# Optimization experiments

Measured on AMD Instinct MI355X. Metric: run time of the kernel, lower is better.

## Reference

```python
import jax, jax.numpy as jnp
import numpy as np

N = 100000      # nodes
E = 1600000     # edges (avg degree 16)
IN = 128
HID = 128
OUT = 128
G = 512         # graphs in batch


def setup_inputs() -> dict:
    key = jax.random.key(0)
    ks = jax.random.split(key, 8)
    x = jax.random.normal(ks[0], (N, IN), dtype=jnp.float32)
    edge_index = jax.random.randint(ks[1], (2, E), 0, N, dtype=jnp.int64)
    batch = jnp.sort(jax.random.randint(ks[2], (N,), 0, G, dtype=jnp.int64))
    # GCNConv params: weight (glorot-ish) + zero bias, per layer
    W1 = jax.random.normal(ks[3], (IN, HID), dtype=jnp.float32) / np.sqrt(IN)
    b1 = jnp.zeros((HID,), jnp.float32)
    W2 = jax.random.normal(ks[4], (HID, OUT), dtype=jnp.float32) / np.sqrt(HID)
    b2 = jnp.zeros((OUT,), jnp.float32)
    return {"x": x, "edge_index": edge_index, "batch": batch,
            "W1": W1, "b1": b1, "W2": W2, "b2": b2}


def _gcn_layer(h, W, b, src, dst, norm, n):
    # linear transform then normalized scatter-add aggregation
    h = h @ W                                  # [N, F_out]
    msg = h[src] * norm[:, None]               # [E+N, F_out]
    out = jax.ops.segment_sum(msg, dst, num_segments=n)
    return out + b


def reference(x, edge_index, batch, W1, b1, W2, b2):
    x = x.astype(jnp.float32)
    n = x.shape[0]
    # GCNConv adds self-loops and uses symmetric deg^-1/2 normalization
    loop = jnp.arange(n)
    src = jnp.concatenate([edge_index[0], loop])
    dst = jnp.concatenate([edge_index[1], loop])
    deg = jax.ops.segment_sum(jnp.ones_like(dst, dtype=x.dtype), dst, num_segments=n)
    dis = jnp.where(deg > 0, jax.lax.rsqrt(jnp.maximum(deg, 1.0)), 0.0)
    norm = dis[src] * dis[dst]                 # [E+N]

    h = jax.nn.relu(_gcn_layer(x, W1, b1, src, dst, norm, n))
    # dropout p=0.0 -> identity
    h = jax.nn.relu(_gcn_layer(h, W2, b2, src, dst, norm, n))

    # global_mean_pool over batch ids
    sums = jax.ops.segment_sum(h, batch, num_segments=G)          # [G, OUT]
    counts = jax.ops.segment_sum(jnp.ones((n,), h.dtype), batch, num_segments=G)
    return sums / jnp.maximum(counts, 1.0)[:, None]
```

## Files before the change

kernel.cpp:

```cpp
#include <hip/hip_runtime.h>
#include <stddef.h>


#define F 128
#define EB 4096
#define BSH 9

typedef unsigned int uint;
typedef unsigned short ushort;
typedef __attribute__((ext_vector_type(8))) short s16x8;
typedef __attribute__((ext_vector_type(4))) float f32x4;

__device__ __forceinline__ float bf_lo(uint v) { return __uint_as_float(v << 16); }
__device__ __forceinline__ float bf_hi(uint v) { return __uint_as_float(v & 0xffff0000u); }
__device__ __forceinline__ ushort f2bf(float f) {
    uint u = __float_as_uint(f);
    u += 0x7fffu + ((u >> 16) & 1u);
    return (ushort)(u >> 16);
}
__device__ __forceinline__ uint pack_bf2(float lo, float hi) {
    return (uint)f2bf(lo) | ((uint)f2bf(hi) << 16);
}

__device__ __forceinline__ int scan256_incl(int* s, int t, int v) {
    s[t] = v;
    __syncthreads();
#pragma unroll
    for (int d = 1; d < 256; d <<= 1) {
        int y = (t >= d) ? s[t - d] : 0;
        __syncthreads();
        s[t] += y;
        __syncthreads();
    }
    return s[t];
}


__global__ __launch_bounds__(256) void passA_kernel(const int* __restrict__ ei,
                                                    int* __restrict__ bucket_cnt,
                                                    int e, int nbuc) {
    __shared__ int h[256];
    int t = threadIdx.x;
    h[t] = 0;
    __syncthreads();
    for (int i = blockIdx.x * 256 + t; i < e; i += gridDim.x * 256)
        atomicAdd(&h[ei[e + i] >> BSH], 1);
    __syncthreads();
    if (t < nbuc && h[t]) atomicAdd(&bucket_cnt[t], h[t]);
}


__global__ __launch_bounds__(256) void prep_scan_kernel(const float* __restrict__ W1,
                                                        const float* __restrict__ W2,
                                                        ushort* __restrict__ wt,
                                                        const int* __restrict__ bucket_cnt,
                                                        int* __restrict__ bucket_base,
                                                        int* __restrict__ gcur, int nbuc) {
    if (blockIdx.x == 128) {
        __shared__ int aux[256];
        int t = threadIdx.x;
        int v = (t < nbuc) ? bucket_cnt[t] : 0;
        int incl = scan256_incl(aux, t, v);
        int base = incl - v;
        bucket_base[t] = base;
        gcur[t] = base;
        if (t == nbuc - 1) bucket_base[nbuc] = incl;
        return;
    }
    int idx = blockIdx.x * 256 + threadIdx.x;
    int m = idx >> 14;
    int c = (idx >> 7) & 127;
    int r = idx & 127;
    const float* W = m ? W2 : W1;
    float w = W[r * F + c];
    ushort hi = f2bf(w);
    float whi = __uint_as_float((uint)hi << 16);
    ushort lo = f2bf(w - whi);
    wt[((m * 2 + 0) * F + c) * F + r] = hi;
    wt[((m * 2 + 1) * F + c) * F + r] = lo;
}


__global__ __launch_bounds__(256) void passB_kernel(const int* __restrict__ ei,
                                                    int* __restrict__ gcur,
                                                    uint2* __restrict__ ebuf, int e) {
    __shared__ uint2 stage[EB];
    __shared__ int h[256], start[256], cur[256], claim[256], aux[256];
    int t = threadIdx.x;
    h[t] = 0;
    __syncthreads();
    int base = blockIdx.x * EB;
    int s_r[16], d_r[16];
#pragma unroll
    for (int k = 0; k < 16; ++k) {
        int i = base + k * 256 + t;
        int sv = -1, dv = 0;
        if (i < e) {
            sv = ei[i];
            dv = ei[e + i];
            atomicAdd(&h[dv >> BSH], 1);
        }
        s_r[k] = sv; d_r[k] = dv;
    }
    __syncthreads();
    int hv = h[t];
    int incl = scan256_incl(aux, t, hv);
    start[t] = incl - hv;
    cur[t]   = incl - hv;
    claim[t] = (hv > 0) ? atomicAdd(&gcur[t], hv) : 0;
    __syncthreads();
#pragma unroll
    for (int k = 0; k < 16; ++k) {
        if (s_r[k] >= 0) {
            int b = d_r[k] >> BSH;
            int r = atomicAdd(&cur[b], 1);
            stage[r] = make_uint2((uint)s_r[k], (uint)d_r[k]);
        }
    }
    __syncthreads();
    int valid = min(EB, e - base);
#pragma unroll
    for (int k = 0; k < 16; ++k) {
        int idx = k * 256 + t;
        if (idx < valid) {
            uint2 ed = stage[idx];
            int b = (int)(ed.y >> BSH);
            ebuf[claim[b] + (idx - start[b])] = ed;
        }
    }
}


__global__ __launch_bounds__(256) void passC1_kernel(const uint2* __restrict__ ebuf,
                                                     const int* __restrict__ bucket_base,
                                                     int* __restrict__ rp,
                                                     float* __restrict__ dis, int n) {
    __shared__ int h[512];
    __shared__ int aux[256];
    int t = threadIdx.x, b = blockIdx.x;
    int v0 = b << BSH;
    h[t] = 0; h[t + 256] = 0;
    __syncthreads();
    int ebeg = bucket_base[b], eend = bucket_base[b + 1];
    for (int i = ebeg + t; i < eend; i += 256)
        atomicAdd(&h[(int)ebuf[i].y - v0], 1);
    __syncthreads();
#pragma unroll
    for (int k = 0; k < 2; ++k) {
        int v = v0 + t + k * 256;
        if (v < n) dis[v] = rsqrtf((float)(h[t + k * 256] + 1));
    }
    int p = h[2 * t] + h[2 * t + 1];
    int incl = scan256_incl(aux, t, p);
    int ex = incl - p;
    int v = v0 + 2 * t;
    if (v <= n)     rp[v]     = ebeg + ex;
    if (v + 1 <= n) rp[v + 1] = ebeg + ex + h[2 * t];
}


__global__ __launch_bounds__(256) void passC2_kernel(const uint2* __restrict__ ebuf,
                                                     const int* __restrict__ bucket_base,
                                                     const int* __restrict__ rp,
                                                     const float* __restrict__ dis,
                                                     uint2* __restrict__ ew, int n) {
    __shared__ int cur[512];
    __shared__ float dl[512];
    int t = threadIdx.x, b = blockIdx.x;
    int v0 = b << BSH;
#pragma unroll
    for (int k = 0; k < 2; ++k) {
        int idx = t + k * 256, v = v0 + idx;
        cur[idx] = (v < n) ? rp[v] : 0;
        dl[idx]  = (v < n) ? dis[v] : 0.f;
    }
    __syncthreads();
    int ebeg = bucket_base[b], eend = bucket_base[b + 1];
    for (int i = ebeg + t; i < eend; i += 256) {
        uint2 ed = ebuf[i];
        int s = (int)ed.x, d = (int)ed.y - v0;
        float w = dis[s] * dl[d];
        int p = atomicAdd(&cur[d], 1);
        ew[p] = make_uint2(ed.x, __float_as_uint(w));
    }
}


template <bool F32IN>
__global__ __launch_bounds__(256) void gemm_mfma_kernel(const float* __restrict__ Af,
                                                        const uint* __restrict__ Ab,
                                                        const ushort* __restrict__ wt,
                                                        ushort* __restrict__ C,
                                                        int n, int nstrips) {
    __shared__ uint4 As4[2][2048];
    const int t = threadIdx.x;
    const int w = t >> 6;
    const int lane = t & 63;
    const int kg = lane >> 4;
    const int lr = lane & 15;

    const uint4* Bg = (const uint4*)wt;
    s16x8 bfr[2][2][4];
#pragma unroll
    for (int part = 0; part < 2; ++part)
#pragma unroll
        for (int c = 0; c < 2; ++c)
#pragma unroll
            for (int ks = 0; ks < 4; ++ks) {
                int col = w * 32 + c * 16 + lr;
                uint4 bu = Bg[part * F * 16 + col * 16 + ks * 4 + kg];
                bfr[part][c][ks] = *(const s16x8*)&bu;
            }

    auto load_strip = [&](int strip, uint4* st) {
        int r0 = strip * 128;
#pragma unroll
        for (int p = 0; p < 8; ++p) {
            int g = p * 256 + t;
            int row = g >> 4, q = g & 15;
            int c8 = q ^ (row & 7);
            uint4 v = make_uint4(0u, 0u, 0u, 0u);
            int gr = r0 + row;
            if (gr < n) {
                if (F32IN) {
                    const float* a = Af + (size_t)gr * F + c8 * 8;
                    float4 f0 = *(const float4*)a;
                    float4 f1 = *(const float4*)(a + 4);
                    v.x = pack_bf2(f0.x, f0.y);
                    v.y = pack_bf2(f0.z, f0.w);
                    v.z = pack_bf2(f1.x, f1.y);
                    v.w = pack_bf2(f1.z, f1.w);
                } else {
                    v = *(const uint4*)(Ab + (size_t)gr * 64 + c8 * 4);
                }
            }
            st[p] = v;
        }
    };

    int s = blockIdx.x;
    if (s >= nstrips) return;
    uint4 st[8];
    load_strip(s, st);
    int buf = 0;
    for (; s < nstrips; s += gridDim.x) {
#pragma unroll
        for (int p = 0; p < 8; ++p) As4[buf][p * 256 + t] = st[p];
        __syncthreads();
        int s2 = s + gridDim.x;
        if (s2 < nstrips) load_strip(s2, st);

        f32x4 acc[8][2];
#pragma unroll
        for (int r = 0; r < 8; ++r)
#pragma unroll
            for (int c = 0; c < 2; ++c) acc[r][c] = (f32x4){0.f, 0.f, 0.f, 0.f};

        const s16x8* As8 = (const s16x8*)As4[buf];
#pragma unroll
        for (int ks = 0; ks < 4; ++ks) {
            s16x8 afr[8];
#pragma unroll
            for (int r = 0; r < 8; ++r) {
                int row = r * 16 + lr;
                afr[r] = As8[row * 16 + ((ks * 4 + kg) ^ (row & 7))];
            }
#pragma unroll
            for (int r = 0; r < 8; ++r)
#pragma unroll
                for (int c = 0; c < 2; ++c) {
                    acc[r][c] = __builtin_amdgcn_mfma_f32_16x16x32_bf16(afr[r], bfr[0][c][ks], acc[r][c], 0, 0, 0);
                    acc[r][c] = __builtin_amdgcn_mfma_f32_16x16x32_bf16(afr[r], bfr[1][c][ks], acc[r][c], 0, 0, 0);
                }
        }
        __syncthreads();

        ushort* Cs = (ushort*)As4[buf];
#pragma unroll
        for (int r = 0; r < 8; ++r)
#pragma unroll
            for (int c = 0; c < 2; ++c)
#pragma unroll
                for (int reg = 0; reg < 4; ++reg) {
                    int row = r * 16 + kg * 4 + reg;
                    int col = w * 32 + c * 16 + lr;
                    Cs[row * F + col] = f2bf(acc[r][c][reg]);
                }
        __syncthreads();
        int r0 = s * 128;
#pragma unroll
        for (int p = 0; p < 8; ++p) {
            int g = p * 256 + t;
            int row = g >> 4, c8 = g & 15;
            if (r0 + row < n)
                *(uint4*)(C + (size_t)(r0 + row) * F + c8 * 8) = As4[buf][g];
        }
        buf ^= 1;
    }
}


__global__ __launch_bounds__(256) void agg_kernel(const uint* __restrict__ h2,
                                                  const int* __restrict__ rp,
                                                  const uint2* __restrict__ ew,
                                                  const float* __restrict__ dis,
                                                  const float* __restrict__ bias,
                                                  uint* __restrict__ out2, int n) {
    int wid = __builtin_amdgcn_readfirstlane(threadIdx.x >> 6);
    int node = blockIdx.x * 4 + wid;
    if (node >= n) return;
    int lane = threadIdx.x & 63;
    float di = dis[node];
    int beg = rp[node], end = rp[node + 1];
    uint hv = h2[((uint)node << 6) | lane];
    float w0 = di * di;
    float ax = w0 * bf_lo(hv);
    float ay = w0 * bf_hi(hv);
    int j = beg;
    for (; j + 16 <= end; j += 16) {
        uint2 E[16];
        uint v[16];
#pragma unroll
        for (int k = 0; k < 16; ++k) E[k] = ew[j + k];
#pragma unroll
        for (int k = 0; k < 16; ++k) v[k] = h2[(E[k].x << 6) | lane];
#pragma unroll
        for (int k = 0; k < 16; ++k) {
            float we = __uint_as_float(E[k].y);
            ax = fmaf(we, bf_lo(v[k]), ax);
            ay = fmaf(we, bf_hi(v[k]), ay);
        }
    }
    for (; j + 4 <= end; j += 4) {
        uint2 E0 = ew[j], E1 = ew[j + 1], E2 = ew[j + 2], E3 = ew[j + 3];
        uint v0 = h2[(E0.x << 6) | lane];
        uint v1 = h2[(E1.x << 6) | lane];
        uint v2 = h2[(E2.x << 6) | lane];
        uint v3 = h2[(E3.x << 6) | lane];
        float w0e = __uint_as_float(E0.y), w1e = __uint_as_float(E1.y);
        float w2e = __uint_as_float(E2.y), w3e = __uint_as_float(E3.y);
        ax = fmaf(w0e, bf_lo(v0), ax); ay = fmaf(w0e, bf_hi(v0), ay);
        ax = fmaf(w1e, bf_lo(v1), ax); ay = fmaf(w1e, bf_hi(v1), ay);
        ax = fmaf(w2e, bf_lo(v2), ax); ay = fmaf(w2e, bf_hi(v2), ay);
        ax = fmaf(w3e, bf_lo(v3), ax); ay = fmaf(w3e, bf_hi(v3), ay);
    }
    for (; j < end; ++j) {
        uint2 E0 = ew[j];
        uint v0 = h2[(E0.x << 6) | lane];
        float w0e = __uint_as_float(E0.y);
        ax = fmaf(w0e, bf_lo(v0), ax);
        ay = fmaf(w0e, bf_hi(v0), ay);
    }
    float2 b = ((const float2*)bias)[lane];
    ax = fmaxf(ax + b.x, 0.f);
    ay = fmaxf(ay + b.y, 0.f);
    out2[((uint)node << 6) | lane] = pack_bf2(ax, ay);
}


__global__ __launch_bounds__(256) void pool_kernel(const uint* __restrict__ h2,
                                                   const int* __restrict__ batch,
                                                   float* __restrict__ out, int n) {
    __shared__ int sb[2];
    __shared__ float red[4][F];
    int g = blockIdx.x;
    int t = threadIdx.x;
    if (t < 2) {
        int target = g + t;
        int lo = 0, hi = n;
        while (lo < hi) {
            int mid = (lo + hi) >> 1;
            if (batch[mid] < target) lo = mid + 1; else hi = mid;
        }
        sb[t] = lo;
    }
    __syncthreads();
    int start = sb[0], end = sb[1];
    int lane = t & 63, w = t >> 6;
    float sx = 0.f, sy = 0.f;
    for (int i = start + w; i < end; i += 4) {
        uint v = h2[((uint)i << 6) | lane];
        sx += bf_lo(v);
        sy += bf_hi(v);
    }
    red[w][lane * 2] = sx;
    red[w][lane * 2 + 1] = sy;
    __syncthreads();
    if (w == 0) {
        float s0 = red[0][lane * 2] + red[1][lane * 2] + red[2][lane * 2] + red[3][lane * 2];
        float s1 = red[0][lane * 2 + 1] + red[1][lane * 2 + 1] + red[2][lane * 2 + 1] + red[3][lane * 2 + 1];
        float inv = 1.f / fmaxf((float)(end - start), 1.f);
        out[(size_t)g * F + lane * 2]     = s0 * inv;
        out[(size_t)g * F + lane * 2 + 1] = s1 * inv;
    }
}


extern "C" void kernel_launch(void* const* d_in, const int* in_sizes, int n_in,
                              void* d_out, int out_size, void* d_ws, size_t ws_size,
                              hipStream_t stream) {
    const float* x     = (const float*)d_in[0];
    const int*   ei    = (const int*)d_in[1];
    const int*   batch = (const int*)d_in[2];
    const float* W1    = (const float*)d_in[3];
    const float* b1    = (const float*)d_in[4];
    const float* W2    = (const float*)d_in[5];
    const float* b2    = (const float*)d_in[6];
    float* out = (float*)d_out;

    const int n = in_sizes[0] / F;
    const int e = in_sizes[1] / 2;
    const int g = out_size / F;
    const int nbuc = (n + (1 << BSH) - 1) >> BSH;

    char* ws = (char*)d_ws;
    size_t off = 0;
    auto alloc = [&](size_t bytes) -> char* {
        char* p = ws + off;
        off += (bytes + 255) & ~(size_t)255;
        return p;
    };
    float*  dis   = (float*)alloc((size_t)n * 4);
    int*    rp    = (int*)  alloc((size_t)(n + 1) * 4);
    int*    bcnt  = (int*)  alloc(256 * 4);
    int*    bbase = (int*)  alloc(257 * 4);
    int*    gcur  = (int*)  alloc(256 * 4);
    uint2*  ebuf  = (uint2*)alloc((size_t)e * 8);
    uint2*  ew    = (uint2*)alloc((size_t)e * 8);
    ushort* wt    = (ushort*)alloc((size_t)4 * F * F * 2);
    uint*   hbuf  = (uint*) alloc((size_t)n * F * 2);
    uint*   abuf  = (uint*) alloc((size_t)n * F * 2);
    (void)ws_size;

    hipMemsetAsync(bcnt, 0, 256 * 4, stream);
    passA_kernel<<<256, 256, 0, stream>>>(ei, bcnt, e, nbuc);
    prep_scan_kernel<<<129, 256, 0, stream>>>(W1, W2, wt, bcnt, bbase, gcur, nbuc);
    passB_kernel<<<(e + EB - 1) / EB, 256, 0, stream>>>(ei, gcur, ebuf, e);
    passC1_kernel<<<nbuc, 256, 0, stream>>>(ebuf, bbase, rp, dis, n);
    passC2_kernel<<<nbuc, 256, 0, stream>>>(ebuf, bbase, rp, dis, ew, n);

    const int nstrips = (n + 127) / 128;
    int ggrid = nstrips < 512 ? nstrips : 512;
    gemm_mfma_kernel<true><<<ggrid, 256, 0, stream>>>(x, nullptr, wt, (ushort*)hbuf, n, nstrips);
    agg_kernel<<<(n + 3) / 4, 256, 0, stream>>>(hbuf, rp, ew, dis, b1, abuf, n);
    gemm_mfma_kernel<false><<<ggrid, 256, 0, stream>>>(nullptr, abuf, wt + 2 * F * F, (ushort*)hbuf, n, nstrips);
    agg_kernel<<<(n + 3) / 4, 256, 0, stream>>>(hbuf, rp, ew, dis, b2, abuf, n);
    pool_kernel<<<g, 256, 0, stream>>>(abuf, batch, out, n);
}
```

Baseline: 349.8 us.

## Pack edge buffer to 32-bit, shrink buckets, one-strip-per-block GEMM

```diff
diff --git a/kernel.cpp b/kernel.cpp
--- a/kernel.cpp
+++ b/kernel.cpp
@@ -4,7 +4,7 @@
 
 #define F 128
 #define EB 4096
-#define BSH 9
+#define BSH 8
 
 typedef unsigned int uint;
 typedef unsigned short ushort;
@@ -39,14 +39,18 @@
 __global__ __launch_bounds__(256) void passA_kernel(const int* __restrict__ ei,
                                                     int* __restrict__ bucket_cnt,
                                                     int e, int nbuc) {
-    __shared__ int h[256];
+    __shared__ int h[512];
     int t = threadIdx.x;
-    h[t] = 0;
+    h[t] = 0; h[t + 256] = 0;
     __syncthreads();
     for (int i = blockIdx.x * 256 + t; i < e; i += gridDim.x * 256)
         atomicAdd(&h[ei[e + i] >> BSH], 1);
     __syncthreads();
-    if (t < nbuc && h[t]) atomicAdd(&bucket_cnt[t], h[t]);
+#pragma unroll
+    for (int k = 0; k < 2; ++k) {
+        int b = t + k * 256;
+        if (b < nbuc && h[b]) atomicAdd(&bucket_cnt[b], h[b]);
+    }
 }
 
 
@@ -59,12 +63,16 @@
     if (blockIdx.x == 128) {
         __shared__ int aux[256];
         int t = threadIdx.x;
-        int v = (t < nbuc) ? bucket_cnt[t] : 0;
-        int incl = scan256_incl(aux, t, v);
-        int base = incl - v;
-        bucket_base[t] = base;
-        gcur[t] = base;
-        if (t == nbuc - 1) bucket_base[nbuc] = incl;
+        int c0 = (2 * t < nbuc) ? bucket_cnt[2 * t] : 0;
+        int c1 = (2 * t + 1 < nbuc) ? bucket_cnt[2 * t + 1] : 0;
+        int p = c0 + c1;
+        int incl = scan256_incl(aux, t, p);
+        int ex = incl - p;
+        bucket_base[2 * t] = ex;
+        bucket_base[2 * t + 1] = ex + c0;
+        gcur[2 * t] = ex;
+        gcur[2 * t + 1] = ex + c0;
+        if (t == 255) bucket_base[512] = incl;
         return;
     }
     int idx = blockIdx.x * 256 + threadIdx.x;
@@ -83,11 +91,11 @@
 
 __global__ __launch_bounds__(256) void passB_kernel(const int* __restrict__ ei,
                                                     int* __restrict__ gcur,
-                                                    uint2* __restrict__ ebuf, int e) {
+                                                    uint* __restrict__ ebuf, int e) {
     __shared__ uint2 stage[EB];
-    __shared__ int h[256], start[256], cur[256], claim[256], aux[256];
+    __shared__ int h[512], start[512], cur[512], claim[512], aux[256];
     int t = threadIdx.x;
-    h[t] = 0;
+    h[t] = 0; h[t + 256] = 0;
     __syncthreads();
     int base = blockIdx.x * EB;
     int s_r[16], d_r[16];
@@ -103,11 +111,16 @@
         s_r[k] = sv; d_r[k] = dv;
     }
     __syncthreads();
-    int hv = h[t];
-    int incl = scan256_incl(aux, t, hv);
-    start[t] = incl - hv;
-    cur[t]   = incl - hv;
-    claim[t] = (hv > 0) ? atomicAdd(&gcur[t], hv) : 0;
+    {
+        int h0 = h[2 * t], h1 = h[2 * t + 1];
+        int p = h0 + h1;
+        int incl = scan256_incl(aux, t, p);
+        int ex = incl - p;
+        start[2 * t] = ex;          start[2 * t + 1] = ex + h0;
+        cur[2 * t] = ex;            cur[2 * t + 1] = ex + h0;
+        claim[2 * t]     = (h0 > 0) ? atomicAdd(&gcur[2 * t], h0) : 0;
+        claim[2 * t + 1] = (h1 > 0) ? atomicAdd(&gcur[2 * t + 1], h1) : 0;
+    }
     __syncthreads();
 #pragma unroll
     for (int k = 0; k < 16; ++k) {
@@ -125,63 +138,58 @@
         if (idx < valid) {
             uint2 ed = stage[idx];
             int b = (int)(ed.y >> BSH);
-            ebuf[claim[b] + (idx - start[b])] = ed;
-        }
-    }
-}
-
-
-__global__ __launch_bounds__(256) void passC1_kernel(const uint2* __restrict__ ebuf,
+            uint dloc = ed.y & ((1u << BSH) - 1u);
+            ebuf[claim[b] + (idx - start[b])] = (dloc << 24) | ed.x;
+        }
+    }
+}
+
+
+__global__ __launch_bounds__(256) void passC1_kernel(const uint* __restrict__ ebuf,
                                                      const int* __restrict__ bucket_base,
                                                      int* __restrict__ rp,
                                                      float* __restrict__ dis, int n) {
-    __shared__ int h[512];
+    __shared__ int h[256];
     __shared__ int aux[256];
     int t = threadIdx.x, b = blockIdx.x;
     int v0 = b << BSH;
-    h[t] = 0; h[t + 256] = 0;
+    h[t] = 0;
     __syncthreads();
     int ebeg = bucket_base[b], eend = bucket_base[b + 1];
     for (int i = ebeg + t; i < eend; i += 256)
-        atomicAdd(&h[(int)ebuf[i].y - v0], 1);
-    __syncthreads();
-#pragma unroll
-    for (int k = 0; k < 2; ++k) {
-        int v = v0 + t + k * 256;
-        if (v < n) dis[v] = rsqrtf((float)(h[t + k * 256] + 1));
-    }
-    int p = h[2 * t] + h[2 * t + 1];
-    int incl = scan256_incl(aux, t, p);
-    int ex = incl - p;
-    int v = v0 + 2 * t;
-    if (v <= n)     rp[v]     = ebeg + ex;
-    if (v + 1 <= n) rp[v + 1] = ebeg + ex + h[2 * t];
-}
-
-
-__global__ __launch_bounds__(256) void passC2_kernel(const uint2* __restrict__ ebuf,
+        atomicAdd(&h[ebuf[i] >> 24], 1);
+    __syncthreads();
+    int cnt = h[t];
+    int v = v0 + t;
+    if (v < n) dis[v] = rsqrtf((float)(cnt + 1));
+    int incl = scan256_incl(aux, t, cnt);
+    int ex = incl - cnt;
+    if (v < n) rp[v] = ebeg + ex;
+    if (v == n - 1) rp[n] = ebeg + incl;
+}
+
+
+__global__ __launch_bounds__(256) void passC2_kernel(const uint* __restrict__ ebuf,
                                                      const int* __restrict__ bucket_base,
                                                      const int* __restrict__ rp,
                                                      const float* __restrict__ dis,
                                                      uint2* __restrict__ ew, int n) {
-    __shared__ int cur[512];
-    __shared__ float dl[512];
+    __shared__ int cur[256];
+    __shared__ float dl[256];
     int t = threadIdx.x, b = blockIdx.x;
     int v0 = b << BSH;
-#pragma unroll
-    for (int k = 0; k < 2; ++k) {
-        int idx = t + k * 256, v = v0 + idx;
-        cur[idx] = (v < n) ? rp[v] : 0;
-        dl[idx]  = (v < n) ? dis[v] : 0.f;
-    }
+    int v = v0 + t;
+    cur[t] = (v < n) ? rp[v] : 0;
+    dl[t]  = (v < n) ? dis[v] : 0.f;
     __syncthreads();
     int ebeg = bucket_base[b], eend = bucket_base[b + 1];
     for (int i = ebeg + t; i < eend; i += 256) {
-        uint2 ed = ebuf[i];
-        int s = (int)ed.x, d = (int)ed.y - v0;
-        float w = dis[s] * dl[d];
+        uint ed = ebuf[i];
+        uint src = ed & 0xFFFFFFu;
+        int d = (int)(ed >> 24);
+        float w = dis[src] * dl[d];
         int p = atomicAdd(&cur[d], 1);
-        ew[p] = make_uint2(ed.x, __float_as_uint(w));
+        ew[p] = make_uint2(src, __float_as_uint(w));
     }
 }
 
@@ -190,14 +198,14 @@
 __global__ __launch_bounds__(256) void gemm_mfma_kernel(const float* __restrict__ Af,
                                                         const uint* __restrict__ Ab,
                                                         const ushort* __restrict__ wt,
-                                                        ushort* __restrict__ C,
-                                                        int n, int nstrips) {
-    __shared__ uint4 As4[2][2048];
+                                                        ushort* __restrict__ C, int n) {
+    __shared__ uint4 As4[2048];
     const int t = threadIdx.x;
     const int w = t >> 6;
     const int lane = t & 63;
     const int kg = lane >> 4;
     const int lr = lane & 15;
+    const int r0 = blockIdx.x * 128;
 
     const uint4* Bg = (const uint4*)wt;
     s16x8 bfr[2][2][4];
@@ -212,90 +220,72 @@
                 bfr[part][c][ks] = *(const s16x8*)&bu;
             }
 
-    auto load_strip = [&](int strip, uint4* st) {
-        int r0 = strip * 128;
-#pragma unroll
-        for (int p = 0; p < 8; ++p) {
-            int g = p * 256 + t;
-            int row = g >> 4, q = g & 15;
-            int c8 = q ^ (row & 7);
-            uint4 v = make_uint4(0u, 0u, 0u, 0u);
-            int gr = r0 + row;
-            if (gr < n) {
-                if (F32IN) {
-                    const float* a = Af + (size_t)gr * F + c8 * 8;
-                    float4 f0 = *(const float4*)a;
-                    float4 f1 = *(const float4*)(a + 4);
-                    v.x = pack_bf2(f0.x, f0.y);
-                    v.y = pack_bf2(f0.z, f0.w);
-                    v.z = pack_bf2(f1.x, f1.y);
-                    v.w = pack_bf2(f1.z, f1.w);
-                } else {
-                    v = *(const uint4*)(Ab + (size_t)gr * 64 + c8 * 4);
-                }
+#pragma unroll
+    for (int p = 0; p < 8; ++p) {
+        int g = p * 256 + t;
+        int row = g >> 4, c8 = g & 15;
+        uint4 v = make_uint4(0u, 0u, 0u, 0u);
+        int gr = r0 + row;
+        if (gr < n) {
+            if (F32IN) {
+                const float* a = Af + (size_t)gr * F + c8 * 8;
+                float4 f0 = *(const float4*)a;
+                float4 f1 = *(const float4*)(a + 4);
+                v.x = pack_bf2(f0.x, f0.y);
+                v.y = pack_bf2(f0.z, f0.w);
+                v.z = pack_bf2(f1.x, f1.y);
+                v.w = pack_bf2(f1.z, f1.w);
+            } else {
+                v = *(const uint4*)(Ab + (size_t)gr * 64 + c8 * 4);
             }
-            st[p] = v;
-        }
-    };
-
-    int s = blockIdx.x;
-    if (s >= nstrips) return;
-    uint4 st[8];
-    load_strip(s, st);
-    int buf = 0;
-    for (; s < nstrips; s += gridDim.x) {
-#pragma unroll
-        for (int p = 0; p < 8; ++p) As4[buf][p * 256 + t] = st[p];
-        __syncthreads();
-        int s2 = s + gridDim.x;
-        if (s2 < nstrips) load_strip(s2, st);
-
-        f32x4 acc[8][2];
+        }
+        As4[row * 16 + (c8 ^ (row & 7))] = v;
+    }
+    __syncthreads();
+
+    f32x4 acc[8][2];
+#pragma unroll
+    for (int r = 0; r < 8; ++r)
+#pragma unroll
+        for (int c = 0; c < 2; ++c) acc[r][c] = (f32x4){0.f, 0.f, 0.f, 0.f};
+
+    const s16x8* As8 = (const s16x8*)As4;
+#pragma unroll
+    for (int ks = 0; ks < 4; ++ks) {
+        s16x8 afr[8];
+#pragma unroll
+        for (int r = 0; r < 8; ++r) {
+            int row = r * 16 + lr;
+            afr[r] = As8[row * 16 + ((ks * 4 + kg) ^ (row & 7))];
+        }
 #pragma unroll
         for (int r = 0; r < 8; ++r)
 #pragma unroll
-            for (int c = 0; c < 2; ++c) acc[r][c] = (f32x4){0.f, 0.f, 0.f, 0.f};
-
-        const s16x8* As8 = (const s16x8*)As4[buf];
-#pragma unroll
-        for (int ks = 0; ks < 4; ++ks) {
-            s16x8 afr[8];
-#pragma unroll
-            for (int r = 0; r < 8; ++r) {
-                int row = r * 16 + lr;
-                afr[r] = As8[row * 16 + ((ks * 4 + kg) ^ (row & 7))];
+            for (int c = 0; c < 2; ++c) {
+                acc[r][c] = __builtin_amdgcn_mfma_f32_16x16x32_bf16(afr[r], bfr[0][c][ks], acc[r][c], 0, 0, 0);
+                acc[r][c] = __builtin_amdgcn_mfma_f32_16x16x32_bf16(afr[r], bfr[1][c][ks], acc[r][c], 0, 0, 0);
             }
-#pragma unroll
-            for (int r = 0; r < 8; ++r)
-#pragma unroll
-                for (int c = 0; c < 2; ++c) {
-                    acc[r][c] = __builtin_amdgcn_mfma_f32_16x16x32_bf16(afr[r], bfr[0][c][ks], acc[r][c], 0, 0, 0);
-                    acc[r][c] = __builtin_amdgcn_mfma_f32_16x16x32_bf16(afr[r], bfr[1][c][ks], acc[r][c], 0, 0, 0);
-                }
-        }
-        __syncthreads();
-
-        ushort* Cs = (ushort*)As4[buf];
-#pragma unroll
-        for (int r = 0; r < 8; ++r)
-#pragma unroll
-            for (int c = 0; c < 2; ++c)
-#pragma unroll
-                for (int reg = 0; reg < 4; ++reg) {
-                    int row = r * 16 + kg * 4 + reg;
-                    int col = w * 32 + c * 16 + lr;
-                    Cs[row * F + col] = f2bf(acc[r][c][reg]);
-                }
-        __syncthreads();
-        int r0 = s * 128;
-#pragma unroll
-        for (int p = 0; p < 8; ++p) {
-            int g = p * 256 + t;
-            int row = g >> 4, c8 = g & 15;
-            if (r0 + row < n)
-                *(uint4*)(C + (size_t)(r0 + row) * F + c8 * 8) = As4[buf][g];
-        }
-        buf ^= 1;
+    }
+    __syncthreads();
+
+    ushort* Cs = (ushort*)As4;
+#pragma unroll
+    for (int r = 0; r < 8; ++r)
+#pragma unroll
+        for (int c = 0; c < 2; ++c)
+#pragma unroll
+            for (int reg = 0; reg < 4; ++reg) {
+                int row = r * 16 + kg * 4 + reg;
+                int col = w * 32 + c * 16 + lr;
+                Cs[row * F + col] = f2bf(acc[r][c][reg]);
+            }
+    __syncthreads();
+#pragma unroll
+    for (int p = 0; p < 8; ++p) {
+        int g = p * 256 + t;
+        int row = g >> 4, c8 = g & 15;
+        if (r0 + row < n)
+            *(uint4*)(C + (size_t)(r0 + row) * F + c8 * 8) = As4[g];
     }
 }
 
@@ -422,17 +412,17 @@
     };
     float*  dis   = (float*)alloc((size_t)n * 4);
     int*    rp    = (int*)  alloc((size_t)(n + 1) * 4);
-    int*    bcnt  = (int*)  alloc(256 * 4);
-    int*    bbase = (int*)  alloc(257 * 4);
-    int*    gcur  = (int*)  alloc(256 * 4);
-    uint2*  ebuf  = (uint2*)alloc((size_t)e * 8);
+    int*    bcnt  = (int*)  alloc(512 * 4);
+    int*    bbase = (int*)  alloc(513 * 4);
+    int*    gcur  = (int*)  alloc(512 * 4);
+    uint*   ebuf  = (uint*) alloc((size_t)e * 4);
     uint2*  ew    = (uint2*)alloc((size_t)e * 8);
     ushort* wt    = (ushort*)alloc((size_t)4 * F * F * 2);
     uint*   hbuf  = (uint*) alloc((size_t)n * F * 2);
     uint*   abuf  = (uint*) alloc((size_t)n * F * 2);
     (void)ws_size;
 
-    hipMemsetAsync(bcnt, 0, 256 * 4, stream);
+    hipMemsetAsync(bcnt, 0, 512 * 4, stream);
     passA_kernel<<<256, 256, 0, stream>>>(ei, bcnt, e, nbuc);
     prep_scan_kernel<<<129, 256, 0, stream>>>(W1, W2, wt, bcnt, bbase, gcur, nbuc);
     passB_kernel<<<(e + EB - 1) / EB, 256, 0, stream>>>(ei, gcur, ebuf, e);
@@ -440,10 +430,9 @@
     passC2_kernel<<<nbuc, 256, 0, stream>>>(ebuf, bbase, rp, dis, ew, n);
 
     const int nstrips = (n + 127) / 128;
-    int ggrid = nstrips < 512 ? nstrips : 512;
-    gemm_mfma_kernel<true><<<ggrid, 256, 0, stream>>>(x, nullptr, wt, (ushort*)hbuf, n, nstrips);
+    gemm_mfma_kernel<true><<<nstrips, 256, 0, stream>>>(x, nullptr, wt, (ushort*)hbuf, n);
     agg_kernel<<<(n + 3) / 4, 256, 0, stream>>>(hbuf, rp, ew, dis, b1, abuf, n);
-    gemm_mfma_kernel<false><<<ggrid, 256, 0, stream>>>(nullptr, abuf, wt + 2 * F * F, (ushort*)hbuf, n, nstrips);
+    gemm_mfma_kernel<false><<<nstrips, 256, 0, stream>>>(nullptr, abuf, wt + 2 * F * F, (ushort*)hbuf, n);
     agg_kernel<<<(n + 3) / 4, 256, 0, stream>>>(hbuf, rp, ew, dis, b2, abuf, n);
     pool_kernel<<<g, 256, 0, stream>>>(abuf, batch, out, n);
 }
```

Result: faster. 338.1 us (-3.4%).
